# Kernel tuning notes

Measured on AMD Instinct MI355X. Metric: run time of the kernel, lower is better.

Reference implementation:

```python
import jax, jax.numpy as jnp
import numpy as np

# Dims (match init_kwargs / module defaults)
RD, PD = 128, 64          # residue_dim, pair_dim
H, QD, VD = 12, 32, 32    # num_heads, q_dim, v_dim
QP, VP = 8, 8             # num_q_points, num_v_points
LN_EPS = 1e-5
DIR_EPS = 1e-4
INF = 1e5


def _layer_norm(x, g, b):
    m = x.mean(-1, keepdims=True)
    v = ((x - m) ** 2).mean(-1, keepdims=True)
    return (x - m) * jax.lax.rsqrt(v + LN_EPS) * g + b


def setup_inputs() -> dict:
    key = jax.random.key(0)
    ks = jax.random.split(key, 24)
    N, L = 2, 512
    inp = {}
    inp['R'] = jax.random.normal(ks[0], (N, L, 3, 3), jnp.float32)
    inp['coord'] = jax.random.normal(ks[1], (N, L, 3), jnp.float32)
    inp['residue_feat'] = jax.random.normal(ks[2], (N, L, RD), jnp.float32)
    inp['pair_feat'] = jax.random.normal(ks[3], (N, L, L, PD), jnp.float32)
    inp['mask'] = jax.random.randint(ks[4], (N, L), 0, 2).astype(bool)

    def lin(k, fan_in, fan_out):  # torch nn.Linear default init, weight (out, in)
        lim = 1.0 / np.sqrt(fan_in)
        return jax.random.uniform(k, (fan_out, fan_in), jnp.float32, -lim, lim)

    inp['Wq'] = lin(ks[5], RD, QD * H)
    inp['Wk'] = lin(ks[6], RD, QD * H)
    inp['Wv'] = lin(ks[7], RD, VD * H)
    inp['Wpb'] = lin(ks[8], PD, H)
    inp['spatial_coef'] = jnp.full((1, 1, 1, H), np.log(np.exp(1.0) - 1.0), jnp.float32)
    inp['Wqp'] = lin(ks[9], RD, QP * H * 3)
    inp['Wkp'] = lin(ks[10], RD, QP * H * 3)
    inp['Wvp'] = lin(ks[11], RD, VP * H * 3)
    in_feat = H * VD + H * PD + H * VP * (3 + 3 + 1)  # 1824
    inp['Wout'] = lin(ks[12], in_feat, RD)
    inp['bout'] = jnp.zeros((RD,), jnp.float32)
    inp['Wm1'] = lin(ks[13], RD, RD)
    inp['bm1'] = jnp.zeros((RD,), jnp.float32)
    inp['Wm2'] = lin(ks[14], RD, RD)
    inp['bm2'] = jnp.zeros((RD,), jnp.float32)
    inp['Wm3'] = lin(ks[15], RD, RD)
    inp['bm3'] = jnp.zeros((RD,), jnp.float32)
    inp['ln1_g'] = jnp.ones((RD,), jnp.float32)
    inp['ln1_b'] = jnp.zeros((RD,), jnp.float32)
    inp['ln2_g'] = jnp.ones((RD,), jnp.float32)
    inp['ln2_b'] = jnp.zeros((RD,), jnp.float32)
    return inp


def _forward(R, coord, residue_feat, pair_feat, mask,
             Wq, Wk, Wv, Wpb, spatial_coef, Wqp, Wkp, Wvp,
             Wout, bout, Wm1, bm1, Wm2, bm2, Wm3, bm3,
             ln1_g, ln1_b, ln2_g, ln2_b):
    N, L, _ = residue_feat.shape

    def l2g(p):  # local->global: R @ p + t ; p: (N,L,M,3)
        return jnp.einsum('nlij,nlmj->nlmi', R, p) + coord[:, :, None, :]

    # --- node logits ---
    q = (residue_feat @ Wq.T).reshape(N, L, H, QD)
    k = (residue_feat @ Wk.T).reshape(N, L, H, QD)
    logits_node = jnp.einsum('nihd,njhd->nijh', q, k) * (1.0 / np.sqrt(QD))

    # --- pair logits ---
    logits_pair = pair_feat @ Wpb.T  # (N,L,L,H)

    # --- spatial logits ---
    qp = l2g((residue_feat @ Wqp.T).reshape(N, L, H * QP, 3)).reshape(N, L, H, QP * 3)
    kp = l2g((residue_feat @ Wkp.T).reshape(N, L, H * QP, 3)).reshape(N, L, H, QP * 3)
    # ||q_i - k_j||^2 = |q|^2 + |k|^2 - 2 q.k (avoids (N,L,L,H,3P) intermediate)
    qq = (qp ** 2).sum(-1)  # (N,L,H)
    kk = (kp ** 2).sum(-1)
    sum_sq = qq[:, :, None] + kk[:, None] - 2.0 * jnp.einsum('nihd,njhd->nijh', qp, kp)
    gamma = jax.nn.softplus(spatial_coef)  # (1,1,1,H)
    logits_spatial = sum_sq * (-gamma * np.sqrt(2.0 / (9.0 * QP)) / 2.0)

    logits = (logits_node + logits_pair + logits_spatial) * np.sqrt(1.0 / 3.0)

    # --- masked softmax over key axis (dim=2) ---
    mask_row = mask[:, :, None, None]            # (N,L,1,1)
    mask_pair = mask_row & mask[:, None, :, None]
    logits = jnp.where(mask_pair, logits, logits - INF)
    alpha = jax.nn.softmax(logits, axis=2)
    alpha = jnp.where(mask_row, alpha, 0.0)      # (N,L,L,H)

    # --- node aggregation ---
    v = (residue_feat @ Wv.T).reshape(N, L, H, VD)
    feat_node = jnp.einsum('nijh,njhd->nihd', alpha, v).reshape(N, L, H * VD)

    # --- pair aggregation ---
    feat_pair = jnp.einsum('nijh,nijc->nihc', alpha, pair_feat).reshape(N, L, H * PD)

    # --- spatial aggregation ---
    vp = l2g((residue_feat @ Wvp.T).reshape(N, L, H * VP, 3)).reshape(N, L, H, VP, 3)
    aggr = jnp.einsum('nijh,njhpc->nihpc', alpha, vp)  # (N,L,H,VP,3) global frame
    diff = aggr - coord[:, :, None, None, :]
    feat_points = jnp.einsum('nlji,nlhpj->nlhpi', R, diff)  # global->local: R^T (x - t)
    feat_dist = jnp.sqrt((feat_points ** 2).sum(-1))        # (N,L,H,VP)
    feat_dir = feat_points / (feat_dist[..., None] + DIR_EPS)
    feat_spatial = jnp.concatenate([
        feat_points.reshape(N, L, -1),
        feat_dist.reshape(N, L, -1),
        feat_dir.reshape(N, L, -1),
    ], axis=-1)

    feat_all = jnp.concatenate([feat_pair, feat_node, feat_spatial], axis=-1)
    feat_all = feat_all @ Wout.T + bout
    feat_all = jnp.where(mask[:, :, None], feat_all, 0.0)

    x = _layer_norm(residue_feat + feat_all, ln1_g, ln1_b)
    mlp = jax.nn.relu(jax.nn.relu(x @ Wm1.T + bm1) @ Wm2.T + bm2) @ Wm3.T + bm3
    return _layer_norm(x + mlp, ln2_g, ln2_b)


def reference(R, coord, residue_feat, pair_feat, mask,
              Wq, Wk, Wv, Wpb, spatial_coef, Wqp, Wkp, Wvp,
              Wout, bout, Wm1, bm1, Wm2, bm2, Wm3, bm3,
              ln1_g, ln1_b, ln2_g, ln2_b):
    return _forward(R, coord, residue_feat, pair_feat, mask,
                    Wq, Wk, Wv, Wpb, spatial_coef, Wqp, Wkp, Wvp,
                    Wout, bout, Wm1, bm1, Wm2, bm2, Wm3, bm3,
                    ln1_g, ln1_b, ln2_g, ln2_b)
```

## Files before the change

kernel.cpp:

```cpp
#include <hip/hip_runtime.h>
#include <hip/hip_bf16.h>

#define N_ 2
#define L_ 512
#define RD_ 128
#define PD_ 64
#define H_ 12
#define NL_ (N_*L_)
#define POUT_ 2016
#define FEAT_ 1824
#define INF_ 100000.0f
#define ISQD_ 0.17677669529663687f
#define ISQ3_ 0.5773502691896258f
#define LL_ ((size_t)L_*L_)

__global__ __launch_bounds__(256) void k_proj_gemm(
    const float* __restrict__ resf,
    const float* __restrict__ Wq, const float* __restrict__ Wk, const float* __restrict__ Wv,
    const float* __restrict__ Wqp, const float* __restrict__ Wkp, const float* __restrict__ Wvp,
    float* __restrict__ proj)
{
  const int rb = blockIdx.x * 8;
  const int ob = blockIdx.y * 128;
  const int tid = threadIdx.x;
  __shared__ float xt[8*132];
  __shared__ float wt[128*132];
  {
    int r = tid >> 5, kq = (tid & 31) * 4;
    float4 v = *(const float4*)(resf + (size_t)(rb + r)*RD_ + kq);
    xt[r*132+kq]=v.x; xt[r*132+kq+1]=v.y; xt[r*132+kq+2]=v.z; xt[r*132+kq+3]=v.w;
  }
  for (int m = 0; m < 16; ++m) {
    int idx = m*256 + tid;
    int r = idx >> 5, kq = (idx & 31) * 4;
    int o = ob + r;
    float4 v;
    if (o < 384)        v = *(const float4*)(Wq  + (size_t)o*RD_ + kq);
    else if (o < 768)   v = *(const float4*)(Wk  + (size_t)(o-384)*RD_ + kq);
    else if (o < 1152)  v = *(const float4*)(Wv  + (size_t)(o-768)*RD_ + kq);
    else if (o < 1440)  v = *(const float4*)(Wqp + (size_t)(o-1152)*RD_ + kq);
    else if (o < 1728)  v = *(const float4*)(Wkp + (size_t)(o-1440)*RD_ + kq);
    else if (o < POUT_) v = *(const float4*)(Wvp + (size_t)(o-1728)*RD_ + kq);
    else                v = make_float4(0.f,0.f,0.f,0.f);
    wt[r*132+kq]=v.x; wt[r*132+kq+1]=v.y; wt[r*132+kq+2]=v.z; wt[r*132+kq+3]=v.w;
  }
  __syncthreads();
  const int tt = tid & 7, g = tid >> 3;
  float acc0=0.f, acc1=0.f, acc2=0.f, acc3=0.f;
  #pragma unroll 4
  for (int k2 = 0; k2 < RD_; k2 += 2) {
    float2 xv = *(const float2*)(xt + tt*132 + k2);
    float2 w0 = *(const float2*)(wt + (g     )*132 + k2);
    float2 w1 = *(const float2*)(wt + (g + 32)*132 + k2);
    float2 w2 = *(const float2*)(wt + (g + 64)*132 + k2);
    float2 w3 = *(const float2*)(wt + (g + 96)*132 + k2);
    acc0 += xv.x*w0.x + xv.y*w0.y;
    acc1 += xv.x*w1.x + xv.y*w1.y;
    acc2 += xv.x*w2.x + xv.y*w2.y;
    acc3 += xv.x*w3.x + xv.y*w3.y;
  }
  float* dst = proj + (size_t)(rb + tt)*POUT_ + ob;
  if (ob + g      < POUT_) dst[g]      = acc0;
  if (ob + g + 32 < POUT_) dst[g+32]   = acc1;
  if (ob + g + 64 < POUT_) dst[g+64]   = acc2;
  if (ob + g + 96 < POUT_) dst[g+96]   = acc3;
}

__global__ __launch_bounds__(64) void k_rot(
    const float* __restrict__ R, const float* __restrict__ coord,
    const float* __restrict__ spc, const float* __restrict__ proj,
    float* __restrict__ qt, float* __restrict__ kt, float* __restrict__ vpg)
{
  const int t = blockIdx.x;
  const int n = t / L_, i = t % L_;
  const int tid = threadIdx.x;
  __shared__ float prow[POUT_];
  __shared__ float qpl[288], kpl[288], vpl[288];
  __shared__ float qqs[H_], kks[H_], coefs[H_];
  for (int m = tid; m < POUT_/4; m += 64)
    ((float4*)prow)[m] = *((const float4*)(proj + (size_t)t*POUT_) + m);
  if (tid < H_) coefs[tid] = -log1pf(expf(spc[tid])) * (1.0f/12.0f);
  __syncthreads();
  const float* Rm = R + (size_t)t*9;
  const float r00=Rm[0],r01=Rm[1],r02=Rm[2],r10=Rm[3],r11=Rm[4],r12=Rm[5],r20=Rm[6],r21=Rm[7],r22=Rm[8];
  const float cx = coord[(size_t)t*3], cy = coord[(size_t)t*3+1], cz = coord[(size_t)t*3+2];
  for (int idx = tid; idx < 288; idx += 64) {
    int mat = idx / 96, p = idx % 96;
    const float* s = prow + 1152 + mat*288 + p*3;
    float px=s[0], py=s[1], pz=s[2];
    float gx = r00*px + r01*py + r02*pz + cx;
    float gy = r10*px + r11*py + r12*pz + cy;
    float gz = r20*px + r21*py + r22*pz + cz;
    float* d = (mat==0? qpl : mat==1? kpl : vpl) + p*3;
    d[0]=gx; d[1]=gy; d[2]=gz;
  }
  __syncthreads();
  if (tid < 24) {
    int mat = tid / H_, h = tid % H_;
    const float* s = (mat==0? qpl : kpl) + h*24;
    float acc = 0.f;
    #pragma unroll
    for (int c2 = 0; c2 < 24; ++c2) acc += s[c2]*s[c2];
    (mat==0? qqs : kks)[h] = acc;
  }
  for (int m = tid; m < 72; m += 64)
    ((float4*)(vpg + (size_t)t*288))[m] = ((float4*)vpl)[m];
  __syncthreads();
  for (int idx = tid; idx < 2*H_*64; idx += 64) {
    int which = idx / 768, rem = idx % 768, h = rem >> 6, c = rem & 63;
    float val;
    if (which == 0) {
      if (c < 32)       val = prow[h*32 + c] * ISQD_;
      else if (c < 56)  val = qpl[h*24 + (c-32)] * (-2.0f * coefs[h]);
      else if (c == 56) val = coefs[h] * qqs[h];
      else if (c == 57) val = coefs[h];
      else              val = 0.f;
      qt[((size_t)(n*H_ + h)*L_ + i)*64 + c] = val;
    } else {
      if (c < 32)       val = prow[384 + h*32 + c];
      else if (c < 56)  val = kpl[h*24 + (c-32)];
      else if (c == 56) val = 1.0f;
      else if (c == 57) val = kks[h];
      else              val = 0.f;
      kt[((size_t)(n*H_ + h)*L_ + i)*64 + c] = val;
    }
  }
}

__global__ __launch_bounds__(256) void k_lgns(
    const float* __restrict__ qt, const float* __restrict__ kt,
    float* __restrict__ lgal)
{
  const int jb = blockIdx.x * 64, ib = blockIdx.y * 64, nh = blockIdx.z;
  const int tid = threadIdx.x;
  __shared__ float qs[64*66], ks[64*66];
  for (int m = 0; m < 4; ++m) {
    int idx = m*256 + tid;
    int r = idx >> 4, kq = (idx & 15) * 4;
    float4 a = *(const float4*)(qt + ((size_t)nh*L_ + ib + r)*64 + kq);
    qs[r*66+kq]=a.x; qs[r*66+kq+1]=a.y; qs[r*66+kq+2]=a.z; qs[r*66+kq+3]=a.w;
    float4 b = *(const float4*)(kt + ((size_t)nh*L_ + jb + r)*64 + kq);
    ks[r*66+kq]=b.x; ks[r*66+kq+1]=b.y; ks[r*66+kq+2]=b.z; ks[r*66+kq+3]=b.w;
  }
  __syncthreads();
  const int tx = tid & 15, ty = tid >> 4;
  const int i0 = ty*4, j0 = tx*4;
  float acc[4][4] = {};
  #pragma unroll 4
  for (int k2 = 0; k2 < 64; k2 += 2) {
    float2 qv[4], kv[4];
    #pragma unroll
    for (int d = 0; d < 4; ++d) {
      qv[d] = *(const float2*)(qs + (i0+d)*66 + k2);
      kv[d] = *(const float2*)(ks + (j0+d)*66 + k2);
    }
    #pragma unroll
    for (int a2 = 0; a2 < 4; ++a2)
      #pragma unroll
      for (int b2 = 0; b2 < 4; ++b2)
        acc[a2][b2] += qv[a2].x*kv[b2].x + qv[a2].y*kv[b2].y;
  }
  #pragma unroll
  for (int a2 = 0; a2 < 4; ++a2) {
    float4 v = make_float4(acc[a2][0], acc[a2][1], acc[a2][2], acc[a2][3]);
    *(float4*)(lgal + ((size_t)nh*L_ + ib + i0 + a2)*L_ + jb + j0) = v;
  }
}

__global__ __launch_bounds__(256) void k_pbsm(
    const float* __restrict__ pair, const int* __restrict__ mask,
    const float* __restrict__ Wpb, float* __restrict__ lgal)
{
  const int i = blockIdx.x, n = blockIdx.y;
  const int bi = n*L_ + i;
  const int tid = threadIdx.x;
  const int l = tid & 63;
  const int w = __builtin_amdgcn_readfirstlane(tid >> 6);
  __shared__ float pt[2][64*67];

  const float* prow = pair + (size_t)bi*L_*PD_;
  const int sr = tid >> 4, scq = (tid & 15)*4;

  #pragma unroll
  for (int m = 0; m < 4; ++m) {
    int r = m*16 + sr;
    float4 v = *(const float4*)(prow + (size_t)r*PD_ + scq);
    float* d = pt[0] + r*67 + scq;
    d[0]=v.x; d[1]=v.y; d[2]=v.z; d[3]=v.w;
  }
  __syncthreads();

  const float* w0 = Wpb + (w    )*64;
  const float* w1 = Wpb + (w + 4)*64;
  const float* w2 = Wpb + (w + 8)*64;
  const int mi = mask[bi];

  float l0[8], l1[8], l2[8];
  const size_t row0 = ((size_t)(n*H_ + w    )*L_ + i)*L_;
  const size_t row1 = ((size_t)(n*H_ + w + 4)*L_ + i)*L_;
  const size_t row2 = ((size_t)(n*H_ + w + 8)*L_ + i)*L_;

  #pragma unroll
  for (int t = 0; t < 8; ++t) {
    float4 rg[4];
    if (t < 7) {
      #pragma unroll
      for (int m = 0; m < 4; ++m) {
        int r = m*16 + sr;
        rg[m] = *(const float4*)(prow + (size_t)((t+1)*64 + r)*PD_ + scq);
      }
    }
    const float* pr = pt[t & 1] + l*67;
    float a0=0.f, a1=0.f, a2=0.f;
    #pragma unroll 16
    for (int c = 0; c < 64; ++c) {
      float pv = pr[c];
      a0 += pv*w0[c]; a1 += pv*w1[c]; a2 += pv*w2[c];
    }
    const int j = t*64 + l;
    const float mt = (mi && mask[n*L_ + j]) ? 0.f : -INF_;
    l0[t] = (lgal[row0 + j] + a0)*ISQ3_ + mt;
    l1[t] = (lgal[row1 + j] + a1)*ISQ3_ + mt;
    l2[t] = (lgal[row2 + j] + a2)*ISQ3_ + mt;
    if (t < 7) {
      __syncthreads();
      #pragma unroll
      for (int m = 0; m < 4; ++m) {
        int r = m*16 + sr;
        float* d = pt[(t+1)&1] + r*67 + scq;
        d[0]=rg[m].x; d[1]=rg[m].y; d[2]=rg[m].z; d[3]=rg[m].w;
      }
      __syncthreads();
    }
  }

  float mx0=-1e30f, mx1=-1e30f, mx2=-1e30f;
  #pragma unroll
  for (int t = 0; t < 8; ++t) {
    mx0 = fmaxf(mx0, l0[t]); mx1 = fmaxf(mx1, l1[t]); mx2 = fmaxf(mx2, l2[t]);
  }
  #pragma unroll
  for (int off = 1; off < 64; off <<= 1) {
    mx0 = fmaxf(mx0, __shfl_xor(mx0, off, 64));
    mx1 = fmaxf(mx1, __shfl_xor(mx1, off, 64));
    mx2 = fmaxf(mx2, __shfl_xor(mx2, off, 64));
  }
  float s0=0.f, s1=0.f, s2=0.f;
  #pragma unroll
  for (int t = 0; t < 8; ++t) {
    l0[t] = expf(l0[t]-mx0); s0 += l0[t];
    l1[t] = expf(l1[t]-mx1); s1 += l1[t];
    l2[t] = expf(l2[t]-mx2); s2 += l2[t];
  }
  #pragma unroll
  for (int off = 1; off < 64; off <<= 1) {
    s0 += __shfl_xor(s0, off, 64);
    s1 += __shfl_xor(s1, off, 64);
    s2 += __shfl_xor(s2, off, 64);
  }
  const float fm = mi ? 1.f : 0.f;
  s0 = fm/s0; s1 = fm/s1; s2 = fm/s2;
  #pragma unroll
  for (int t = 0; t < 8; ++t) {
    const int j = t*64 + l;
    lgal[row0 + j] = l0[t]*s0;
    lgal[row1 + j] = l1[t]*s1;
    lgal[row2 + j] = l2[t]*s2;
  }
}

__global__ __launch_bounds__(256) void k_paggr(
    const float* __restrict__ pair, const float* __restrict__ lgal,
    float* __restrict__ feat)
{
  const int i = blockIdx.x, n = blockIdx.y;
  const int bi = n*L_ + i;
  const int tid = threadIdx.x;
  const int w = tid >> 6, l = tid & 63;
  const int js = l >> 4, cq = (l & 15) << 2;
  __shared__ float part[4][H_][64];

  const float* prow = pair + (size_t)bi*L_*PD_;
  const float* arow = lgal + ((size_t)(n*H_)*L_ + i)*L_;

  float4 acc[H_];
  #pragma unroll
  for (int h = 0; h < H_; ++h) acc[h] = make_float4(0.f,0.f,0.f,0.f);

  for (int g = 0; g < 8; ++g) {
    const int j0 = w*128 + g*16 + js*4;
    float4 pv0 = *(const float4*)(prow + (size_t)(j0  )*PD_ + cq);
    float4 pv1 = *(const float4*)(prow + (size_t)(j0+1)*PD_ + cq);
    float4 pv2 = *(const float4*)(prow + (size_t)(j0+2)*PD_ + cq);
    float4 pv3 = *(const float4*)(prow + (size_t)(j0+3)*PD_ + cq);
    #pragma unroll
    for (int h = 0; h < H_; ++h) {
      float4 a4 = *(const float4*)(arow + (size_t)h*LL_ + j0);
      acc[h].x += a4.x*pv0.x + a4.y*pv1.x + a4.z*pv2.x + a4.w*pv3.x;
      acc[h].y += a4.x*pv0.y + a4.y*pv1.y + a4.z*pv2.y + a4.w*pv3.y;
      acc[h].z += a4.x*pv0.z + a4.y*pv1.z + a4.z*pv2.z + a4.w*pv3.z;
      acc[h].w += a4.x*pv0.w + a4.y*pv1.w + a4.z*pv2.w + a4.w*pv3.w;
    }
  }

  #pragma unroll
  for (int h = 0; h < H_; ++h) {
    acc[h].x += __shfl_xor(acc[h].x, 16, 64);
    acc[h].y += __shfl_xor(acc[h].y, 16, 64);
    acc[h].z += __shfl_xor(acc[h].z, 16, 64);
    acc[h].w += __shfl_xor(acc[h].w, 16, 64);
    acc[h].x += __shfl_xor(acc[h].x, 32, 64);
    acc[h].y += __shfl_xor(acc[h].y, 32, 64);
    acc[h].z += __shfl_xor(acc[h].z, 32, 64);
    acc[h].w += __shfl_xor(acc[h].w, 32, 64);
  }
  if (l < 16) {
    #pragma unroll
    for (int h = 0; h < H_; ++h)
      *(float4*)(&part[w][h][cq]) = acc[h];
  }
  __syncthreads();
  for (int u = tid; u < H_*64; u += 256) {
    int h = u >> 6, c = u & 63;
    feat[(size_t)bi*FEAT_ + h*64 + c] =
        part[0][h][c] + part[1][h][c] + part[2][h][c] + part[3][h][c];
  }
}

__global__ __launch_bounds__(256) void k_av(
    const float* __restrict__ lgal, const float* __restrict__ proj,
    const float* __restrict__ vpg, float* __restrict__ pav)
{
  const int ib = blockIdx.x * 64;
  const int nh = blockIdx.y;
  const int z  = blockIdx.z;
  const int jb = z*64;
  const int n = nh / H_, h = nh % H_, nL = n*L_;
  const int tid = threadIdx.x;
  __shared__ float as[64*66];
  __shared__ float bs[64*60];
  const int tx = tid & 15, ty = tid >> 4;
  const int i0 = ty*4, c0 = tx*4;
  for (int m = 0; m < 4; ++m) {
    int idx = m*256 + tid;
    int r = idx >> 4, jq = (idx & 15) * 4;
    float4 a = *(const float4*)(lgal + ((size_t)nh*L_ + ib + r)*L_ + jb + jq);
    as[r*66+jq]=a.x; as[r*66+jq+1]=a.y; as[r*66+jq+2]=a.z; as[r*66+jq+3]=a.w;
  }
  for (int m = 0; m < 4; ++m) {
    int idx = m*256 + tid;
    int j = idx >> 4, qq = idx & 15;
    if (qq < 14) {
      float4 v;
      if (qq < 8) v = *(const float4*)(proj + (size_t)(nL + jb + j)*POUT_ + 768 + h*32 + qq*4);
      else        v = *(const float4*)(vpg  + (size_t)(nL + jb + j)*288  + h*24 + (qq-8)*4);
      float* d = bs + j*60 + qq*4;
      d[0]=v.x; d[1]=v.y; d[2]=v.z; d[3]=v.w;
    }
  }
  __syncthreads();
  float acc[4][4] = {};
  #pragma unroll 4
  for (int k2 = 0; k2 < 64; k2 += 2) {
    float2 av[4];
    #pragma unroll
    for (int d = 0; d < 4; ++d) av[d] = *(const float2*)(as + (i0+d)*66 + k2);
    float4 bv0 = *(const float4*)(bs + (k2  )*60 + c0);
    float4 bv1 = *(const float4*)(bs + (k2+1)*60 + c0);
    #pragma unroll
    for (int a2 = 0; a2 < 4; ++a2) {
      acc[a2][0] += av[a2].x*bv0.x + av[a2].y*bv1.x;
      acc[a2][1] += av[a2].x*bv0.y + av[a2].y*bv1.y;
      acc[a2][2] += av[a2].x*bv0.z + av[a2].y*bv1.z;
      acc[a2][3] += av[a2].x*bv0.w + av[a2].y*bv1.w;
    }
  }
  if (c0 < 56) {
    #pragma unroll
    for (int a2 = 0; a2 < 4; ++a2)
      *(float4*)(pav + (((size_t)z*24 + nh)*L_ + ib + i0 + a2)*56 + c0) =
          make_float4(acc[a2][0], acc[a2][1], acc[a2][2], acc[a2][3]);
  }
}

__global__ __launch_bounds__(256) void k_avred(
    const float* __restrict__ pav, const float* __restrict__ R,
    const float* __restrict__ coord, float* __restrict__ feat)
{
  const int tok = blockIdx.x, tid = threadIdx.x;
  const int n = tok / L_, i = tok % L_;
  __shared__ float ag[288];
  float* fb = feat + (size_t)tok*FEAT_;
  const size_t zstride = (size_t)24*L_*56;
  for (int u = tid; u < 672; u += 256) {
    int h = u / 56, c = u % 56;
    size_t base = (((size_t)(n*H_ + h))*L_ + i)*56 + c;
    float v = 0.f;
    #pragma unroll
    for (int zz = 0; zz < 8; ++zz) v += pav[base + zz*zstride];
    if (c < 32) fb[768 + h*32 + c] = v;
    else        ag[h*24 + (c - 32)] = v;
  }
  __syncthreads();
  if (tid < 96) {
    const float* Rm = R + (size_t)tok*9;
    const float cx = coord[(size_t)tok*3], cy = coord[(size_t)tok*3+1], cz = coord[(size_t)tok*3+2];
    float dx = ag[tid*3] - cx, dy = ag[tid*3+1] - cy, dz = ag[tid*3+2] - cz;
    float fx = Rm[0]*dx + Rm[3]*dy + Rm[6]*dz;
    float fy = Rm[1]*dx + Rm[4]*dy + Rm[7]*dz;
    float fz = Rm[2]*dx + Rm[5]*dy + Rm[8]*dz;
    float dist = sqrtf(fx*fx + fy*fy + fz*fz);
    float idn = 1.f/(dist + 1e-4f);
    fb[1152+tid*3]=fx; fb[1152+tid*3+1]=fy; fb[1152+tid*3+2]=fz;
    fb[1440+tid]=dist;
    fb[1536+tid*3]=fx*idn; fb[1536+tid*3+1]=fy*idn; fb[1536+tid*3+2]=fz*idn;
  }
}

__global__ __launch_bounds__(256) void k_y_gemm(
    const float* __restrict__ feat, const float* __restrict__ Wout,
    float* __restrict__ ybuf)
{
  const int rb = blockIdx.x * 8;
  const int ob = blockIdx.y * 64;
  const int tid = threadIdx.x;
  __shared__ float wt[96*65];
  __shared__ float ft[96*10];
  const int o = tid & 63, tg = tid >> 6;
  float acc0 = 0.f, acc1 = 0.f;
  for (int kb = 0; kb < FEAT_; kb += 96) {
    for (int m = 0; m < 6; ++m) {
      int idx = m*256 + tid;
      int r = idx / 24, cq = (idx % 24) * 4;
      float4 v = *(const float4*)(Wout + (size_t)(ob + r)*FEAT_ + kb + cq);
      wt[(cq  )*65 + r] = v.x;
      wt[(cq+1)*65 + r] = v.y;
      wt[(cq+2)*65 + r] = v.z;
      wt[(cq+3)*65 + r] = v.w;
    }
    if (tid < 192) {
      int t = tid / 24, cq = (tid % 24) * 4;
      float4 v = *(const float4*)(feat + (size_t)(rb + t)*FEAT_ + kb + cq);
      ft[(cq  )*10 + t] = v.x;
      ft[(cq+1)*10 + t] = v.y;
      ft[(cq+2)*10 + t] = v.z;
      ft[(cq+3)*10 + t] = v.w;
    }
    __syncthreads();
    #pragma unroll 4
    for (int k2 = 0; k2 < 96; ++k2) {
      float wv = wt[k2*65 + o];
      float2 fv = *(const float2*)(ft + k2*10 + tg*2);
      acc0 += wv * fv.x;
      acc1 += wv * fv.y;
    }
    __syncthreads();
  }
  ybuf[(size_t)(rb + tg*2    )*RD_ + ob + o] = acc0;
  ybuf[(size_t)(rb + tg*2 + 1)*RD_ + ob + o] = acc1;
}

__device__ __forceinline__ float bsum128(float v, float* red, int tid) {
  #pragma unroll
  for (int off = 1; off < 64; off <<= 1) v += __shfl_xor(v, off, 64);
  __syncthreads();
  if ((tid & 63) == 0) red[tid >> 6] = v;
  __syncthreads();
  return red[0] + red[1];
}

__global__ __launch_bounds__(128) void k_mlp(
    const float* __restrict__ resf, const int* __restrict__ mask,
    const float* __restrict__ ybuf, const float* __restrict__ bout,
    const float* __restrict__ Wm1, const float* __restrict__ bm1,
    const float* __restrict__ Wm2, const float* __restrict__ bm2,
    const float* __restrict__ Wm3, const float* __restrict__ bm3,
    const float* __restrict__ g1, const float* __restrict__ b1,
    const float* __restrict__ g2, const float* __restrict__ b2,
    float* __restrict__ out)
{
  const int t = blockIdx.x, tid = threadIdx.x;
  __shared__ float xb[RD_], h1b[RD_], h2b[RD_];
  __shared__ float red[2];
  float acc = ybuf[(size_t)t*RD_ + tid] + bout[tid];
  if (mask[t] == 0) acc = 0.f;
  float r = resf[(size_t)t*RD_ + tid] + acc;

  float mean = bsum128(r, red, tid) * (1.f/RD_);
  float d = r - mean;
  float var = bsum128(d*d, red, tid) * (1.f/RD_);
  float xn = d * rsqrtf(var + 1e-5f) * g1[tid] + b1[tid];
  xb[tid] = xn;
  __syncthreads();

  float a1 = bm1[tid];
  {
    const float4* w4 = (const float4*)(Wm1 + (size_t)tid*RD_);
    #pragma unroll
    for (int c = 0; c < RD_/4; ++c) { float4 a = w4[c]; a1 += a.x*xb[4*c]+a.y*xb[4*c+1]+a.z*xb[4*c+2]+a.w*xb[4*c+3]; }
  }
  a1 = fmaxf(a1, 0.f);
  h1b[tid] = a1;
  __syncthreads();

  float a2 = bm2[tid];
  {
    const float4* w4 = (const float4*)(Wm2 + (size_t)tid*RD_);
    #pragma unroll
    for (int c = 0; c < RD_/4; ++c) { float4 a = w4[c]; a2 += a.x*h1b[4*c]+a.y*h1b[4*c+1]+a.z*h1b[4*c+2]+a.w*h1b[4*c+3]; }
  }
  a2 = fmaxf(a2, 0.f);
  h2b[tid] = a2;
  __syncthreads();

  float a3 = bm3[tid];
  {
    const float4* w4 = (const float4*)(Wm3 + (size_t)tid*RD_);
    #pragma unroll
    for (int c = 0; c < RD_/4; ++c) { float4 a = w4[c]; a3 += a.x*h2b[4*c]+a.y*h2b[4*c+1]+a.z*h2b[4*c+2]+a.w*h2b[4*c+3]; }
  }
  float r2 = xn + a3;
  float mean2 = bsum128(r2, red, tid) * (1.f/RD_);
  float d2 = r2 - mean2;
  float var2 = bsum128(d2*d2, red, tid) * (1.f/RD_);
  out[(size_t)t*RD_ + tid] = d2 * rsqrtf(var2 + 1e-5f) * g2[tid] + b2[tid];
}

extern "C" void kernel_launch(void* const* d_in, const int* in_sizes, int n_in,
                              void* d_out, int out_size, void* d_ws, size_t ws_size,
                              hipStream_t stream) {
  (void)in_sizes; (void)n_in; (void)out_size; (void)ws_size;
  const float* R     = (const float*)d_in[0];
  const float* coord = (const float*)d_in[1];
  const float* resf  = (const float*)d_in[2];
  const float* pair  = (const float*)d_in[3];
  const int*   mask  = (const int*)  d_in[4];
  const float* Wq    = (const float*)d_in[5];
  const float* Wk    = (const float*)d_in[6];
  const float* Wv    = (const float*)d_in[7];
  const float* Wpb   = (const float*)d_in[8];
  const float* spc   = (const float*)d_in[9];
  const float* Wqp   = (const float*)d_in[10];
  const float* Wkp   = (const float*)d_in[11];
  const float* Wvp   = (const float*)d_in[12];
  const float* Wout  = (const float*)d_in[13];
  const float* bout  = (const float*)d_in[14];
  const float* Wm1   = (const float*)d_in[15];
  const float* bm1   = (const float*)d_in[16];
  const float* Wm2   = (const float*)d_in[17];
  const float* bm2   = (const float*)d_in[18];
  const float* Wm3   = (const float*)d_in[19];
  const float* bm3   = (const float*)d_in[20];
  const float* g1    = (const float*)d_in[21];
  const float* b1    = (const float*)d_in[22];
  const float* g2    = (const float*)d_in[23];
  const float* b2    = (const float*)d_in[24];

  float* ws   = (float*)d_ws;
  float* proj = ws;
  float* qt   = proj + (size_t)NL_*POUT_;
  float* kt   = qt   + (size_t)N_*H_*L_*64;
  float* vpg  = kt   + (size_t)N_*H_*L_*64;
  float* lgal = vpg  + (size_t)NL_*288;
  float* feat = lgal + (size_t)N_*H_*L_*L_;
  float* ybuf = feat + (size_t)NL_*FEAT_;
  float* pav  = ybuf + (size_t)NL_*RD_;

  k_proj_gemm<<<dim3(NL_/8, 16), 256, 0, stream>>>(resf, Wq, Wk, Wv, Wqp, Wkp, Wvp, proj);
  k_rot<<<NL_, 64, 0, stream>>>(R, coord, spc, proj, qt, kt, vpg);
  k_lgns<<<dim3(L_/64, L_/64, N_*H_), 256, 0, stream>>>(qt, kt, lgal);
  k_pbsm<<<dim3(L_, N_), 256, 0, stream>>>(pair, mask, Wpb, lgal);
  k_paggr<<<dim3(L_, N_), 256, 0, stream>>>(pair, lgal, feat);
  k_av<<<dim3(L_/64, N_*H_, 8), 256, 0, stream>>>(lgal, proj, vpg, pav);
  k_avred<<<NL_, 256, 0, stream>>>(pav, R, coord, feat);
  k_y_gemm<<<dim3(NL_/8, 2), 256, 0, stream>>>(feat, Wout, ybuf);
  k_mlp<<<NL_, 128, 0, stream>>>(resf, mask, ybuf, bout, Wm1, bm1, Wm2, bm2, Wm3, bm3,
                                 g1, b1, g2, b2, (float*)d_out);
}
```

Before: 247.5 us.

## Fuse pair aggregation into softmax kernel and batch four tokens per MLP block

```diff
diff --git a/kernel.cpp b/kernel.cpp
--- a/kernel.cpp
+++ b/kernel.cpp
@@ -169,14 +169,17 @@
 
 __global__ __launch_bounds__(256) void k_pbsm(
     const float* __restrict__ pair, const int* __restrict__ mask,
-    const float* __restrict__ Wpb, float* __restrict__ lgal)
+    const float* __restrict__ Wpb, float* __restrict__ lgal,
+    float* __restrict__ feat)
 {
   const int i = blockIdx.x, n = blockIdx.y;
   const int bi = n*L_ + i;
   const int tid = threadIdx.x;
   const int l = tid & 63;
   const int w = __builtin_amdgcn_readfirstlane(tid >> 6);
-  __shared__ float pt[2][64*67];
+  __shared__ float smem[9264];
+  float* pt0 = smem;
+  float* pt1 = smem + 64*66;
 
   const float* prow = pair + (size_t)bi*L_*PD_;
   const int sr = tid >> 4, scq = (tid & 15)*4;
@@ -185,7 +188,7 @@
   for (int m = 0; m < 4; ++m) {
     int r = m*16 + sr;
     float4 v = *(const float4*)(prow + (size_t)r*PD_ + scq);
-    float* d = pt[0] + r*67 + scq;
+    float* d = pt0 + r*66 + scq;
     d[0]=v.x; d[1]=v.y; d[2]=v.z; d[3]=v.w;
   }
   __syncthreads();
@@ -210,12 +213,17 @@
         rg[m] = *(const float4*)(prow + (size_t)((t+1)*64 + r)*PD_ + scq);
       }
     }
-    const float* pr = pt[t & 1] + l*67;
+    const float* pr = (t & 1 ? pt1 : pt0) + l*66;
     float a0=0.f, a1=0.f, a2=0.f;
-    #pragma unroll 16
-    for (int c = 0; c < 64; ++c) {
-      float pv = pr[c];
-      a0 += pv*w0[c]; a1 += pv*w1[c]; a2 += pv*w2[c];
+    #pragma unroll
+    for (int c = 0; c < 64; c += 2) {
+      float2 pv = *(const float2*)(pr + c);
+      float2 u0 = *(const float2*)(w0 + c);
+      float2 u1 = *(const float2*)(w1 + c);
+      float2 u2 = *(const float2*)(w2 + c);
+      a0 += pv.x*u0.x + pv.y*u0.y;
+      a1 += pv.x*u1.x + pv.y*u1.y;
+      a2 += pv.x*u2.x + pv.y*u2.y;
     }
     const int j = t*64 + l;
     const float mt = (mi && mask[n*L_ + j]) ? 0.f : -INF_;
@@ -224,10 +232,11 @@
     l2[t] = (lgal[row2 + j] + a2)*ISQ3_ + mt;
     if (t < 7) {
       __syncthreads();
+      float* dpt = (t & 1 ? pt0 : pt1);
       #pragma unroll
       for (int m = 0; m < 4; ++m) {
         int r = m*16 + sr;
-        float* d = pt[(t+1)&1] + r*67 + scq;
+        float* d = dpt + r*66 + scq;
         d[0]=rg[m].x; d[1]=rg[m].y; d[2]=rg[m].z; d[3]=rg[m].w;
       }
       __syncthreads();
@@ -260,70 +269,63 @@
   }
   const float fm = mi ? 1.f : 0.f;
   s0 = fm/s0; s1 = fm/s1; s2 = fm/s2;
+
+  __syncthreads();
+  float* alf  = smem;
+  float* part = smem + 12*516;
   #pragma unroll
   for (int t = 0; t < 8; ++t) {
     const int j = t*64 + l;
-    lgal[row0 + j] = l0[t]*s0;
-    lgal[row1 + j] = l1[t]*s1;
-    lgal[row2 + j] = l2[t]*s2;
-  }
-}
-
-__global__ __launch_bounds__(256) void k_paggr(
-    const float* __restrict__ pair, const float* __restrict__ lgal,
-    float* __restrict__ feat)
-{
-  const int i = blockIdx.x, n = blockIdx.y;
-  const int bi = n*L_ + i;
-  const int tid = threadIdx.x;
-  const int w = tid >> 6, l = tid & 63;
-  const int js = l >> 4, cq = (l & 15) << 2;
-  __shared__ float part[4][H_][64];
-
-  const float* prow = pair + (size_t)bi*L_*PD_;
-  const float* arow = lgal + ((size_t)(n*H_)*L_ + i)*L_;
-
-  float4 acc[H_];
-  #pragma unroll
-  for (int h = 0; h < H_; ++h) acc[h] = make_float4(0.f,0.f,0.f,0.f);
-
-  for (int g = 0; g < 8; ++g) {
-    const int j0 = w*128 + g*16 + js*4;
-    float4 pv0 = *(const float4*)(prow + (size_t)(j0  )*PD_ + cq);
-    float4 pv1 = *(const float4*)(prow + (size_t)(j0+1)*PD_ + cq);
-    float4 pv2 = *(const float4*)(prow + (size_t)(j0+2)*PD_ + cq);
-    float4 pv3 = *(const float4*)(prow + (size_t)(j0+3)*PD_ + cq);
+    float a0v = l0[t]*s0, a1v = l1[t]*s1, a2v = l2[t]*s2;
+    lgal[row0 + j] = a0v;  alf[(w    )*516 + j] = a0v;
+    lgal[row1 + j] = a1v;  alf[(w + 4)*516 + j] = a1v;
+    lgal[row2 + j] = a2v;  alf[(w + 8)*516 + j] = a2v;
+  }
+  __syncthreads();
+
+  {
+    const int js = l >> 4, cq = (l & 15) << 2;
+    float4 acc[H_];
+    #pragma unroll
+    for (int h = 0; h < H_; ++h) acc[h] = make_float4(0.f,0.f,0.f,0.f);
+    for (int g = 0; g < 8; ++g) {
+      const int j0 = w*128 + g*16 + js*4;
+      float4 pv0 = *(const float4*)(prow + (size_t)(j0  )*PD_ + cq);
+      float4 pv1 = *(const float4*)(prow + (size_t)(j0+1)*PD_ + cq);
+      float4 pv2 = *(const float4*)(prow + (size_t)(j0+2)*PD_ + cq);
+      float4 pv3 = *(const float4*)(prow + (size_t)(j0+3)*PD_ + cq);
+      #pragma unroll
+      for (int h = 0; h < H_; ++h) {
+        float4 a4 = *(const float4*)(alf + h*516 + j0);
+        acc[h].x += a4.x*pv0.x + a4.y*pv1.x + a4.z*pv2.x + a4.w*pv3.x;
+        acc[h].y += a4.x*pv0.y + a4.y*pv1.y + a4.z*pv2.y + a4.w*pv3.y;
+        acc[h].z += a4.x*pv0.z + a4.y*pv1.z + a4.z*pv2.z + a4.w*pv3.z;
+        acc[h].w += a4.x*pv0.w + a4.y*pv1.w + a4.z*pv2.w + a4.w*pv3.w;
+      }
+    }
     #pragma unroll
     for (int h = 0; h < H_; ++h) {
-      float4 a4 = *(const float4*)(arow + (size_t)h*LL_ + j0);
-      acc[h].x += a4.x*pv0.x + a4.y*pv1.x + a4.z*pv2.x + a4.w*pv3.x;
-      acc[h].y += a4.x*pv0.y + a4.y*pv1.y + a4.z*pv2.y + a4.w*pv3.y;
-      acc[h].z += a4.x*pv0.z + a4.y*pv1.z + a4.z*pv2.z + a4.w*pv3.z;
-      acc[h].w += a4.x*pv0.w + a4.y*pv1.w + a4.z*pv2.w + a4.w*pv3.w;
-    }
-  }
-
-  #pragma unroll
-  for (int h = 0; h < H_; ++h) {
-    acc[h].x += __shfl_xor(acc[h].x, 16, 64);
-    acc[h].y += __shfl_xor(acc[h].y, 16, 64);
-    acc[h].z += __shfl_xor(acc[h].z, 16, 64);
-    acc[h].w += __shfl_xor(acc[h].w, 16, 64);
-    acc[h].x += __shfl_xor(acc[h].x, 32, 64);
-    acc[h].y += __shfl_xor(acc[h].y, 32, 64);
-    acc[h].z += __shfl_xor(acc[h].z, 32, 64);
-    acc[h].w += __shfl_xor(acc[h].w, 32, 64);
-  }
-  if (l < 16) {
-    #pragma unroll
-    for (int h = 0; h < H_; ++h)
-      *(float4*)(&part[w][h][cq]) = acc[h];
-  }
-  __syncthreads();
-  for (int u = tid; u < H_*64; u += 256) {
-    int h = u >> 6, c = u & 63;
-    feat[(size_t)bi*FEAT_ + h*64 + c] =
-        part[0][h][c] + part[1][h][c] + part[2][h][c] + part[3][h][c];
+      acc[h].x += __shfl_xor(acc[h].x, 16, 64);
+      acc[h].y += __shfl_xor(acc[h].y, 16, 64);
+      acc[h].z += __shfl_xor(acc[h].z, 16, 64);
+      acc[h].w += __shfl_xor(acc[h].w, 16, 64);
+      acc[h].x += __shfl_xor(acc[h].x, 32, 64);
+      acc[h].y += __shfl_xor(acc[h].y, 32, 64);
+      acc[h].z += __shfl_xor(acc[h].z, 32, 64);
+      acc[h].w += __shfl_xor(acc[h].w, 32, 64);
+    }
+    if (l < 16) {
+      #pragma unroll
+      for (int h = 0; h < H_; ++h)
+        *(float4*)(part + w*768 + h*64 + cq) = acc[h];
+    }
+    __syncthreads();
+    for (int u = tid; u < H_*64; u += 256) {
+      int h = u >> 6, c = u & 63;
+      feat[(size_t)bi*FEAT_ + h*64 + c] =
+          part[0*768 + h*64 + c] + part[1*768 + h*64 + c] +
+          part[2*768 + h*64 + c] + part[3*768 + h*64 + c];
+    }
   }
 }
 
@@ -460,16 +462,7 @@
   ybuf[(size_t)(rb + tg*2 + 1)*RD_ + ob + o] = acc1;
 }
 
-__device__ __forceinline__ float bsum128(float v, float* red, int tid) {
-  #pragma unroll
-  for (int off = 1; off < 64; off <<= 1) v += __shfl_xor(v, off, 64);
-  __syncthreads();
-  if ((tid & 63) == 0) red[tid >> 6] = v;
-  __syncthreads();
-  return red[0] + red[1];
-}
-
-__global__ __launch_bounds__(128) void k_mlp(
+__global__ __launch_bounds__(256) void k_mlp(
     const float* __restrict__ resf, const int* __restrict__ mask,
     const float* __restrict__ ybuf, const float* __restrict__ bout,
     const float* __restrict__ Wm1, const float* __restrict__ bm1,
@@ -479,51 +472,107 @@
     const float* __restrict__ g2, const float* __restrict__ b2,
     float* __restrict__ out)
 {
-  const int t = blockIdx.x, tid = threadIdx.x;
-  __shared__ float xb[RD_], h1b[RD_], h2b[RD_];
-  __shared__ float red[2];
-  float acc = ybuf[(size_t)t*RD_ + tid] + bout[tid];
-  if (mask[t] == 0) acc = 0.f;
-  float r = resf[(size_t)t*RD_ + tid] + acc;
-
-  float mean = bsum128(r, red, tid) * (1.f/RD_);
-  float d = r - mean;
-  float var = bsum128(d*d, red, tid) * (1.f/RD_);
-  float xn = d * rsqrtf(var + 1e-5f) * g1[tid] + b1[tid];
-  xb[tid] = xn;
-  __syncthreads();
-
-  float a1 = bm1[tid];
+  const int t0 = blockIdx.x*4, tid = threadIdx.x;
+  const int tg = tid >> 7, o = tid & 127;
+  const int wid = tid >> 6, lane = tid & 63;
+  const int ta = t0 + tg*2, tb = ta + 1;
+  __shared__ float xb[4][132], hb[4][132];
+  __shared__ float reda[4], redb[4];
+
+  float va = ybuf[(size_t)ta*RD_ + o] + bout[o];
+  float vb = ybuf[(size_t)tb*RD_ + o] + bout[o];
+  if (mask[ta] == 0) va = 0.f;
+  if (mask[tb] == 0) vb = 0.f;
+  float ra = resf[(size_t)ta*RD_ + o] + va;
+  float rb = resf[(size_t)tb*RD_ + o] + vb;
+
+  float pa = ra, pb = rb;
+  #pragma unroll
+  for (int off = 1; off < 64; off <<= 1) { pa += __shfl_xor(pa, off, 64); pb += __shfl_xor(pb, off, 64); }
+  if (lane == 0) { reda[wid] = pa; redb[wid] = pb; }
+  __syncthreads();
+  float mean_a = (reda[2*tg] + reda[2*tg+1]) * (1.f/RD_);
+  float mean_b = (redb[2*tg] + redb[2*tg+1]) * (1.f/RD_);
+  __syncthreads();
+  float da = ra - mean_a, db = rb - mean_b;
+  pa = da*da; pb = db*db;
+  #pragma unroll
+  for (int off = 1; off < 64; off <<= 1) { pa += __shfl_xor(pa, off, 64); pb += __shfl_xor(pb, off, 64); }
+  if (lane == 0) { reda[wid] = pa; redb[wid] = pb; }
+  __syncthreads();
+  float var_a = (reda[2*tg] + reda[2*tg+1]) * (1.f/RD_);
+  float var_b = (redb[2*tg] + redb[2*tg+1]) * (1.f/RD_);
+  float xna = da * rsqrtf(var_a + 1e-5f) * g1[o] + b1[o];
+  float xnb = db * rsqrtf(var_b + 1e-5f) * g1[o] + b1[o];
+  xb[tg*2  ][o] = xna;
+  xb[tg*2+1][o] = xnb;
+  __syncthreads();
+
+  float a1a = bm1[o], a1b = a1a;
   {
-    const float4* w4 = (const float4*)(Wm1 + (size_t)tid*RD_);
-    #pragma unroll
-    for (int c = 0; c < RD_/4; ++c) { float4 a = w4[c]; a1 += a.x*xb[4*c]+a.y*xb[4*c+1]+a.z*xb[4*c+2]+a.w*xb[4*c+3]; }
-  }
-  a1 = fmaxf(a1, 0.f);
-  h1b[tid] = a1;
-  __syncthreads();
-
-  float a2 = bm2[tid];
+    const float4* w4 = (const float4*)(Wm1 + (size_t)o*RD_);
+    #pragma unroll
+    for (int c = 0; c < RD_/4; ++c) {
+      float4 wv = w4[c];
+      float4 xa = *(const float4*)(&xb[tg*2  ][4*c]);
+      float4 xv = *(const float4*)(&xb[tg*2+1][4*c]);
+      a1a += wv.x*xa.x + wv.y*xa.y + wv.z*xa.z + wv.w*xa.w;
+      a1b += wv.x*xv.x + wv.y*xv.y + wv.z*xv.z + wv.w*xv.w;
+    }
+  }
+  a1a = fmaxf(a1a, 0.f); a1b = fmaxf(a1b, 0.f);
+  hb[tg*2][o] = a1a; hb[tg*2+1][o] = a1b;
+  __syncthreads();
+
+  float a2a = bm2[o], a2b = a2a;
   {
-    const float4* w4 = (const float4*)(Wm2 + (size_t)tid*RD_);
-    #pragma unroll
-    for (int c = 0; c < RD_/4; ++c) { float4 a = w4[c]; a2 += a.x*h1b[4*c]+a.y*h1b[4*c+1]+a.z*h1b[4*c+2]+a.w*h1b[4*c+3]; }
-  }
-  a2 = fmaxf(a2, 0.f);
-  h2b[tid] = a2;
-  __syncthreads();
-
-  float a3 = bm3[tid];
+    const float4* w4 = (const float4*)(Wm2 + (size_t)o*RD_);
+    #pragma unroll
+    for (int c = 0; c < RD_/4; ++c) {
+      float4 wv = w4[c];
+      float4 xa = *(const float4*)(&hb[tg*2  ][4*c]);
+      float4 xv = *(const float4*)(&hb[tg*2+1][4*c]);
+      a2a += wv.x*xa.x + wv.y*xa.y + wv.z*xa.z + wv.w*xa.w;
+      a2b += wv.x*xv.x + wv.y*xv.y + wv.z*xv.z + wv.w*xv.w;
+    }
+  }
+  a2a = fmaxf(a2a, 0.f); a2b = fmaxf(a2b, 0.f);
+  __syncthreads();
+  hb[tg*2][o] = a2a; hb[tg*2+1][o] = a2b;
+  __syncthreads();
+
+  float a3a = bm3[o], a3b = a3a;
   {
-    const float4* w4 = (const float4*)(Wm3 + (size_t)tid*RD_);
-    #pragma unroll
-    for (int c = 0; c < RD_/4; ++c) { float4 a = w4[c]; a3 += a.x*h2b[4*c]+a.y*h2b[4*c+1]+a.z*h2b[4*c+2]+a.w*h2b[4*c+3]; }
-  }
-  float r2 = xn + a3;
-  float mean2 = bsum128(r2, red, tid) * (1.f/RD_);
-  float d2 = r2 - mean2;
-  float var2 = bsum128(d2*d2, red, tid) * (1.f/RD_);
-  out[(size_t)t*RD_ + tid] = d2 * rsqrtf(var2 + 1e-5f) * g2[tid] + b2[tid];
+    const float4* w4 = (const float4*)(Wm3 + (size_t)o*RD_);
+    #pragma unroll
+    for (int c = 0; c < RD_/4; ++c) {
+      float4 wv = w4[c];
+      float4 xa = *(const float4*)(&hb[tg*2  ][4*c]);
+      float4 xv = *(const float4*)(&hb[tg*2+1][4*c]);
+      a3a += wv.x*xa.x + wv.y*xa.y + wv.z*xa.z + wv.w*xa.w;
+      a3b += wv.x*xv.x + wv.y*xv.y + wv.z*xv.z + wv.w*xv.w;
+    }
+  }
+  float r2a = xna + a3a, r2b = xnb + a3b;
+
+  pa = r2a; pb = r2b;
+  #pragma unroll
+  for (int off = 1; off < 64; off <<= 1) { pa += __shfl_xor(pa, off, 64); pb += __shfl_xor(pb, off, 64); }
+  if (lane == 0) { reda[wid] = pa; redb[wid] = pb; }
+  __syncthreads();
+  float m2a = (reda[2*tg] + reda[2*tg+1]) * (1.f/RD_);
+  float m2b = (redb[2*tg] + redb[2*tg+1]) * (1.f/RD_);
+  __syncthreads();
+  float d2a = r2a - m2a, d2b = r2b - m2b;
+  pa = d2a*d2a; pb = d2b*d2b;
+  #pragma unroll
+  for (int off = 1; off < 64; off <<= 1) { pa += __shfl_xor(pa, off, 64); pb += __shfl_xor(pb, off, 64); }
+  if (lane == 0) { reda[wid] = pa; redb[wid] = pb; }
+  __syncthreads();
+  float v2a = (reda[2*tg] + reda[2*tg+1]) * (1.f/RD_);
+  float v2b = (redb[2*tg] + redb[2*tg+1]) * (1.f/RD_);
+  out[(size_t)ta*RD_ + o] = d2a * rsqrtf(v2a + 1e-5f) * g2[o] + b2[o];
+  out[(size_t)tb*RD_ + o] = d2b * rsqrtf(v2b + 1e-5f) * g2[o] + b2[o];
 }
 
 extern "C" void kernel_launch(void* const* d_in, const int* in_sizes, int n_in,
@@ -569,11 +618,10 @@
   k_proj_gemm<<<dim3(NL_/8, 16), 256, 0, stream>>>(resf, Wq, Wk, Wv, Wqp, Wkp, Wvp, proj);
   k_rot<<<NL_, 64, 0, stream>>>(R, coord, spc, proj, qt, kt, vpg);
   k_lgns<<<dim3(L_/64, L_/64, N_*H_), 256, 0, stream>>>(qt, kt, lgal);
-  k_pbsm<<<dim3(L_, N_), 256, 0, stream>>>(pair, mask, Wpb, lgal);
-  k_paggr<<<dim3(L_, N_), 256, 0, stream>>>(pair, lgal, feat);
+  k_pbsm<<<dim3(L_, N_), 256, 0, stream>>>(pair, mask, Wpb, lgal, feat);
   k_av<<<dim3(L_/64, N_*H_, 8), 256, 0, stream>>>(lgal, proj, vpg, pav);
   k_avred<<<NL_, 256, 0, stream>>>(pav, R, coord, feat);
   k_y_gemm<<<dim3(NL_/8, 2), 256, 0, stream>>>(feat, Wout, ybuf);
-  k_mlp<<<NL_, 128, 0, stream>>>(resf, mask, ybuf, bout, Wm1, bm1, Wm2, bm2, Wm3, bm3,
-                                 g1, b1, g2, b2, (float*)d_out);
-}
+  k_mlp<<<NL_/4, 256, 0, stream>>>(resf, mask, ybuf, bout, Wm1, bm1, Wm2, bm2, Wm3, bm3,
+                                   g1, b1, g2, b2, (float*)d_out);
+}
```

After: 311.0 us. 1.26x slower.
